# Kernel tuning notes

Hardware: AMD Instinct MI355X
Metric: run time of the kernel (lower is better)

The kernel has to match this reference:

```python
import math
import jax, jax.numpy as jnp
import numpy as np

KERNEL_SIZE = 5
SIGMA = 2.0
# scipy.ndimage.gaussian_filter(5, sigma=2) on a 0-d array returns 5.0 unchanged,
# so the 'gaussian_kernel' is effectively this scalar constant.
GK = 5.0 * math.sqrt(2.0 * math.pi) * SIGMA * SIGMA
EPS = 1e-06


def setup_inputs() -> dict:
    key = jax.random.key(0)
    k1, k2, k3 = jax.random.split(key, 3)
    B, C, H, W = 16, 3, 1024, 1024
    grad_h = jax.random.normal(k1, (B, C, H, W), dtype=jnp.float32)
    grad_w = jax.random.normal(k2, (B, C, H, W), dtype=jnp.float32)
    gam = jax.random.uniform(k3, (B, 1, 1), dtype=jnp.float32)
    return {"grad_h": grad_h, "grad_w": grad_w, "gam": gam}


def _box_sum(x):
    # 5x5 valid sliding-window sum over the spatial dims of NCHW input.
    # Equivalent to torch: unfold(k=5) -> sum over the 25 patch elements,
    # but computed directly without the im2col blowup.
    return jax.lax.reduce_window(
        x, 0.0, jax.lax.add,
        window_dimensions=(1, 1, KERNEL_SIZE, KERNEL_SIZE),
        window_strides=(1, 1, 1, 1),
        padding='VALID')


def reference(grad_h, grad_w, gam):
    B, C = grad_h.shape[0], grad_h.shape[1]
    # lx = |gk * window_sum(grad)| ; dx = gk * window_sum(|grad|)
    lx = jnp.abs(GK * _box_sum(grad_h)).reshape(B, C, -1)   # [B,C,L]
    dx = (GK * _box_sum(jnp.abs(grad_h))).reshape(B, C, -1)
    ly = jnp.abs(GK * _box_sum(grad_w)).reshape(B, C, -1)
    dy = (GK * _box_sum(jnp.abs(grad_w))).reshape(B, C, -1)
    w = jnp.exp(1.0 - gam)  # [B,1,1] broadcasts over [B,C,L]
    norm_loss = (dx / (lx + EPS) * w).mean() + (dy / (ly + EPS) * w).mean()
    return norm_loss
```

## Files before the change

kernel.cpp:

```cpp
#include <hip/hip_runtime.h>
#include <math.h>

#define HH 1024
#define WW 1024
#define OH 1020
#define OW 1020
#define KS 5
#define CHUNK 64
#define NCHUNK 16
#define TPB 256
#define T 4
#define NIMG 48
#define CCH 3

#define GKC 50.132565492620004f
#define EPSC 1e-6f
#define RECOMP_T 1e-4f

__device__ __forceinline__ float win25_np(const float* __restrict__ p) {
    float s = 0.0f;
    #pragma unroll
    for (int r = 0; r < KS; ++r) {
        const float* q = p + (size_t)r * WW;
        float t = q[0];
        t += q[1]; t += q[2]; t += q[3]; t += q[4];
        s += t;
    }
    return s;
}

__device__ __forceinline__ void load_row(const float* __restrict__ row,
                                         float* __restrict__ s,
                                         float* __restrict__ a) {
    float4 u = *reinterpret_cast<const float4*>(row);
    float4 v = *reinterpret_cast<const float4*>(row + 4);
    float s0 = ((u.x + u.y) + (u.z + u.w)) + v.x;
    s[0] = s0;
    s[1] = s0   - u.x + v.y;
    s[2] = s[1] - u.y + v.z;
    s[3] = s[2] - u.z + v.w;
    float p0 = fabsf(u.x), p1 = fabsf(u.y), p2 = fabsf(u.z), p3 = fabsf(u.w);
    float q0 = fabsf(v.x), q1 = fabsf(v.y), q2 = fabsf(v.z), q3 = fabsf(v.w);
    float t0 = ((p0 + p1) + (p2 + p3)) + q0;
    a[0] = t0;
    a[1] = t0   - p0 + q1;
    a[2] = a[1] - p1 + q2;
    a[3] = a[2] - p2 + q3;
}

__global__ __launch_bounds__(TPB)
void rtv_partial(const float* __restrict__ gh, const float* __restrict__ gw,
                 const float* __restrict__ gam, double* __restrict__ partial)
{
    const int x0  = (int)threadIdx.x * T;
    const int img = blockIdx.z;
    const int y0  = blockIdx.y * CHUNK;
    const int y1  = min(y0 + CHUNK, OH);

    float acc = 0.0f;

    if (x0 < OW) {
        const float* __restrict__ ph = gh + (size_t)img * HH * WW;
        const float* __restrict__ pw = gw + (size_t)img * HH * WW;

        float hs[KS][T], ha[KS][T], vws[KS][T], vwa[KS][T];
        #pragma unroll
        for (int i = 0; i < KS - 1; ++i) {
            load_row(ph + (size_t)(y0 + i) * WW + x0, hs[i], ha[i]);
            load_row(pw + (size_t)(y0 + i) * WW + x0, vws[i], vwa[i]);
        }

        for (int yb = y0; yb < y1; yb += KS) {
            #pragma unroll
            for (int k = 0; k < KS; ++k) {
                const int y = yb + k;
                if (y < y1) {
                    const int snew = (k + 4) % KS;
                    load_row(ph + (size_t)(y + 4) * WW + x0, hs[snew], ha[snew]);
                    load_row(pw + (size_t)(y + 4) * WW + x0, vws[snew], vwa[snew]);

                    #pragma unroll
                    for (int j = 0; j < T; ++j) {
                        float vs_h = ((hs[k % KS][j] + hs[(k + 1) % KS][j])
                                    + (hs[(k + 2) % KS][j] + hs[(k + 3) % KS][j]))
                                    +  hs[(k + 4) % KS][j];
                        float va_h = ((ha[k % KS][j] + ha[(k + 1) % KS][j])
                                    + (ha[(k + 2) % KS][j] + ha[(k + 3) % KS][j]))
                                    +  ha[(k + 4) % KS][j];
                        float vs_w = ((vws[k % KS][j] + vws[(k + 1) % KS][j])
                                    + (vws[(k + 2) % KS][j] + vws[(k + 3) % KS][j]))
                                    +  vws[(k + 4) % KS][j];
                        float va_w = ((vwa[k % KS][j] + vwa[(k + 1) % KS][j])
                                    + (vwa[(k + 2) % KS][j] + vwa[(k + 3) % KS][j]))
                                    +  vwa[(k + 4) % KS][j];

                        float den_h, den_w;
                        if (__builtin_expect(fabsf(vs_h) < RECOMP_T, 0)) {
                            float s32 = win25_np(ph + (size_t)y * WW + x0 + j);
                            den_h = fabsf(GKC * s32) + EPSC;
                        } else {
                            den_h = fabsf(GKC * vs_h) + EPSC;
                        }
                        if (__builtin_expect(fabsf(vs_w) < RECOMP_T, 0)) {
                            float s32 = win25_np(pw + (size_t)y * WW + x0 + j);
                            den_w = fabsf(GKC * s32) + EPSC;
                        } else {
                            den_w = fabsf(GKC * vs_w) + EPSC;
                        }

                        acc += (GKC * va_h) * __builtin_amdgcn_rcpf(den_h)
                             + (GKC * va_w) * __builtin_amdgcn_rcpf(den_w);
                    }
                }
            }
        }
    }

    const int b = img / CCH;
    double accd = (double)acc * (double)expf(1.0f - gam[b]);

    #pragma unroll
    for (int off = 32; off >= 1; off >>= 1)
        accd += __shfl_down(accd, off, 64);

    __shared__ double red[TPB / 64];
    const int lane = threadIdx.x & 63;
    const int wid  = threadIdx.x >> 6;
    if (lane == 0) red[wid] = accd;
    __syncthreads();
    if (threadIdx.x == 0) {
        double t = (red[0] + red[1]) + (red[2] + red[3]);
        partial[(size_t)blockIdx.z * gridDim.y + blockIdx.y] = t;
    }
}

__global__ __launch_bounds__(256)
void rtv_reduce(const double* __restrict__ partial, int n,
                float* __restrict__ out)
{
    double acc = 0.0;
    for (int i = threadIdx.x; i < n; i += 256)
        acc += partial[i];

    #pragma unroll
    for (int off = 32; off >= 1; off >>= 1)
        acc += __shfl_down(acc, off, 64);

    __shared__ double red[4];
    const int lane = threadIdx.x & 63;
    const int wid  = threadIdx.x >> 6;
    if (lane == 0) red[wid] = acc;
    __syncthreads();
    if (threadIdx.x == 0) {
        double tot = (red[0] + red[1]) + (red[2] + red[3]);
        const double N = 48.0 * 1040400.0;
        out[0] = (float)(tot / N);
    }
}

extern "C" void kernel_launch(void* const* d_in, const int* in_sizes, int n_in,
                              void* d_out, int out_size, void* d_ws, size_t ws_size,
                              hipStream_t stream) {
    const float* gh  = (const float*)d_in[0];
    const float* gw  = (const float*)d_in[1];
    const float* gam = (const float*)d_in[2];
    float* out = (float*)d_out;
    double* ws = (double*)d_ws;

    dim3 grid(1, NCHUNK, NIMG);
    rtv_partial<<<grid, TPB, 0, stream>>>(gh, gw, gam, ws);

    const int nparts = NCHUNK * NIMG;
    rtv_reduce<<<1, 256, 0, stream>>>(ws, nparts, out);
}
```

Measured before the change: 101.9 us.

## Split fused h/w stencil into two sequential passes and halve row chunk

Processes grad_h and grad_w in two separate passes per thread instead of interleaving both in one loop. This halves the live register footprint of the sliding-window state and should allow higher occupancy. The row chunk is also halved, doubling the number of blocks for more parallelism. In exchange, the 4-row halo reloads per chunk rise in proportion to the rows processed, and each pass has fewer independent loads in flight.

```diff
diff --git a/kernel.cpp b/kernel.cpp
--- a/kernel.cpp
+++ b/kernel.cpp
@@ -6,8 +6,8 @@
 #define OH 1020
 #define OW 1020
 #define KS 5
-#define CHUNK 64
-#define NCHUNK 16
+#define CHUNK 32
+#define NCHUNK 32
 #define TPB 256
 #define T 4
 #define NIMG 48
@@ -48,6 +48,48 @@
     a[3] = a[2] - p2 + q3;
 }
 
+__device__ __forceinline__ float pass_one(const float* __restrict__ p,
+                                          int x0, int y0, int y1) {
+    float hs[KS][T], ha[KS][T];
+    #pragma unroll
+    for (int i = 0; i < KS - 1; ++i)
+        load_row(p + (size_t)(y0 + i) * WW + x0, hs[i], ha[i]);
+
+    float acc = 0.0f;
+    for (int yb = y0; yb < y1; yb += KS) {
+        #pragma unroll
+        for (int k = 0; k < KS; ++k) {
+            const int y = yb + k;
+            if (y < y1) {
+                const int snew = (k + 4) % KS;
+                load_row(p + (size_t)(y + 4) * WW + x0, hs[snew], ha[snew]);
+
+                float r[T];
+                #pragma unroll
+                for (int j = 0; j < T; ++j) {
+                    float vs = ((hs[k % KS][j] + hs[(k + 1) % KS][j])
+                              + (hs[(k + 2) % KS][j] + hs[(k + 3) % KS][j]))
+                              +  hs[(k + 4) % KS][j];
+                    float va = ((ha[k % KS][j] + ha[(k + 1) % KS][j])
+                              + (ha[(k + 2) % KS][j] + ha[(k + 3) % KS][j]))
+                              +  ha[(k + 4) % KS][j];
+
+                    float den;
+                    if (__builtin_expect(fabsf(vs) < RECOMP_T, 0)) {
+                        float s32 = win25_np(p + (size_t)y * WW + x0 + j);
+                        den = fabsf(GKC * s32) + EPSC;
+                    } else {
+                        den = fabsf(GKC * vs) + EPSC;
+                    }
+                    r[j] = (GKC * va) * __builtin_amdgcn_rcpf(den);
+                }
+                acc += (r[0] + r[1]) + (r[2] + r[3]);
+            }
+        }
+    }
+    return acc;
+}
+
 __global__ __launch_bounds__(TPB)
 void rtv_partial(const float* __restrict__ gh, const float* __restrict__ gw,
                  const float* __restrict__ gam, double* __restrict__ partial)
@@ -57,67 +99,17 @@
     const int y0  = blockIdx.y * CHUNK;
     const int y1  = min(y0 + CHUNK, OH);
 
-    float acc = 0.0f;
-
+    float acc_h = 0.0f, acc_w = 0.0f;
     if (x0 < OW) {
         const float* __restrict__ ph = gh + (size_t)img * HH * WW;
         const float* __restrict__ pw = gw + (size_t)img * HH * WW;
-
-        float hs[KS][T], ha[KS][T], vws[KS][T], vwa[KS][T];
-        #pragma unroll
-        for (int i = 0; i < KS - 1; ++i) {
-            load_row(ph + (size_t)(y0 + i) * WW + x0, hs[i], ha[i]);
-            load_row(pw + (size_t)(y0 + i) * WW + x0, vws[i], vwa[i]);
-        }
-
-        for (int yb = y0; yb < y1; yb += KS) {
-            #pragma unroll
-            for (int k = 0; k < KS; ++k) {
-                const int y = yb + k;
-                if (y < y1) {
-                    const int snew = (k + 4) % KS;
-                    load_row(ph + (size_t)(y + 4) * WW + x0, hs[snew], ha[snew]);
-                    load_row(pw + (size_t)(y + 4) * WW + x0, vws[snew], vwa[snew]);
-
-                    #pragma unroll
-                    for (int j = 0; j < T; ++j) {
-                        float vs_h = ((hs[k % KS][j] + hs[(k + 1) % KS][j])
-                                    + (hs[(k + 2) % KS][j] + hs[(k + 3) % KS][j]))
-                                    +  hs[(k + 4) % KS][j];
-                        float va_h = ((ha[k % KS][j] + ha[(k + 1) % KS][j])
-                                    + (ha[(k + 2) % KS][j] + ha[(k + 3) % KS][j]))
-                                    +  ha[(k + 4) % KS][j];
-                        float vs_w = ((vws[k % KS][j] + vws[(k + 1) % KS][j])
-                                    + (vws[(k + 2) % KS][j] + vws[(k + 3) % KS][j]))
-                                    +  vws[(k + 4) % KS][j];
-                        float va_w = ((vwa[k % KS][j] + vwa[(k + 1) % KS][j])
-                                    + (vwa[(k + 2) % KS][j] + vwa[(k + 3) % KS][j]))
-                                    +  vwa[(k + 4) % KS][j];
-
-                        float den_h, den_w;
-                        if (__builtin_expect(fabsf(vs_h) < RECOMP_T, 0)) {
-                            float s32 = win25_np(ph + (size_t)y * WW + x0 + j);
-                            den_h = fabsf(GKC * s32) + EPSC;
-                        } else {
-                            den_h = fabsf(GKC * vs_h) + EPSC;
-                        }
-                        if (__builtin_expect(fabsf(vs_w) < RECOMP_T, 0)) {
-                            float s32 = win25_np(pw + (size_t)y * WW + x0 + j);
-                            den_w = fabsf(GKC * s32) + EPSC;
-                        } else {
-                            den_w = fabsf(GKC * vs_w) + EPSC;
-                        }
-
-                        acc += (GKC * va_h) * __builtin_amdgcn_rcpf(den_h)
-                             + (GKC * va_w) * __builtin_amdgcn_rcpf(den_w);
-                    }
-                }
-            }
-        }
+        acc_h = pass_one(ph, x0, y0, y1);
+        acc_w = pass_one(pw, x0, y0, y1);
     }
 
     const int b = img / CCH;
-    double accd = (double)acc * (double)expf(1.0f - gam[b]);
+    double accd = ((double)acc_h + (double)acc_w)
+                * (double)expf(1.0f - gam[b]);
 
     #pragma unroll
     for (int off = 32; off >= 1; off >>= 1)
```

After: 121.2 us. +18.9%, slower.
